# Kernel optimization log

Measured on AMD Instinct MI355X. Metric: run time of the kernel, lower is better.

The kernel has to match this reference:

```python
import jax, jax.numpy as jnp
import numpy as np

B, N, T, FH, H = 4, 5000, 12, 12, 128
DEG = 16
BN = B * N


def setup_inputs():
    key = jax.random.key(0)
    ks = jax.random.split(key, 12)
    rng = np.random.default_rng(0)
    e = N * DEG
    s = rng.integers(0, N, size=(B, e))
    d = rng.integers(0, N, size=(B, e))
    off = (np.arange(B) * N)[:, None]
    edge_index = jnp.asarray(np.stack([(s + off).ravel(), (d + off).ravel()]), dtype=jnp.int32)

    def lin(k, i, o):
        return jax.random.normal(k, (i, o), jnp.float32) / np.sqrt(i).astype(np.float32)

    return {
        "x": jax.random.normal(ks[0], (B, N, T), jnp.float32),
        "gcn_w1": lin(ks[1], 1, 64), "gcn_b1": jnp.zeros(64),
        "gcn_w2": lin(ks[2], 64, H), "gcn_b2": jnp.zeros(H),
        "gcn_w3": lin(ks[3], H, H), "gcn_b3": jnp.zeros(H),
        "att_w1": lin(ks[4], H, H), "att_b1": jnp.zeros(H),
        "att_w2": lin(ks[5], H, 1), "att_b2": jnp.zeros(1),
        "gru_w_ih": jax.random.normal(ks[6], (3 * H, H), jnp.float32) / np.sqrt(H).astype(np.float32),
        "gru_w_hh": jax.random.normal(ks[7], (3 * H, H), jnp.float32) / np.sqrt(H).astype(np.float32),
        "gru_b_ih": jnp.zeros(3 * H), "gru_b_hh": jnp.zeros(3 * H),
        "ode_w1": lin(ks[8], H, H), "ode_b1": jnp.zeros(H),
        "ode_w2": lin(ks[9], H, H), "ode_b2": jnp.zeros(H),
        "out_w": lin(ks[10], H, 1), "out_b": jnp.zeros(1),
        "edge_index": edge_index,
    }


def _forward(x, gcn_w1, gcn_b1, gcn_w2, gcn_b2, gcn_w3, gcn_b3,
             att_w1, att_b1, att_w2, att_b2,
             gru_w_ih, gru_w_hh, gru_b_ih, gru_b_hh,
             ode_w1, ode_b1, ode_w2, ode_b2, out_w, out_b, edge_index):
    # GCNConv with added self-loops and symmetric normalization (PyG semantics)
    loops = jnp.arange(BN, dtype=edge_index.dtype)
    src = jnp.concatenate([edge_index[0], loops])
    dst = jnp.concatenate([edge_index[1], loops])
    deg = jnp.zeros(BN, x.dtype).at[dst].add(1.0)  # >= 1 thanks to self-loops
    dinv = jax.lax.rsqrt(deg)
    norm = (dinv[src] * dinv[dst])[:, None]  # (E+BN, 1)

    def gcn(h, W, b):
        h = h @ W  # (BN, out)
        agg = jnp.zeros((BN, W.shape[1]), h.dtype).at[dst].add(h[src] * norm)
        return agg + b

    # spatial encoder per timestep (scan over the small time axis)
    x_steps = x.reshape(BN, T).T[:, :, None]  # (T, BN, 1)

    def spatial_step(_, x_t):
        h = jax.nn.relu(gcn(x_t, gcn_w1, gcn_b1))
        h = jax.nn.relu(gcn(h, gcn_w2, gcn_b2))
        h = jax.nn.relu(gcn(h, gcn_w3, gcn_b3))
        return None, h

    _, h_seq = jax.lax.scan(spatial_step, None, x_steps)  # (T, BN, H)
    h_seq = h_seq.reshape(T, B, N, H).transpose(1, 0, 2, 3)  # (B, T, N, H)

    # temporal attention over time axis
    att = jnp.tanh(h_seq @ att_w1 + att_b1) @ att_w2 + att_b2  # (B, T, N, 1)
    aw = jax.nn.softmax(att, axis=1)
    node_features = jnp.sum(h_seq * aw, axis=1).reshape(BN, H)

    # single-step GRU with zero initial hidden (torch gate order r, z, n)
    h0 = jnp.zeros((BN, H), x.dtype)
    gi = node_features @ gru_w_ih.T + gru_b_ih
    gh = h0 @ gru_w_hh.T + gru_b_hh
    ir, iz, inn = jnp.split(gi, 3, axis=1)
    hr, hz, hn = jnp.split(gh, 3, axis=1)
    r = jax.nn.sigmoid(ir + hr)
    z = jax.nn.sigmoid(iz + hz)
    n = jnp.tanh(inn + r * hn)
    hidden = (1.0 - z) * n + z * h0  # (BN, H)

    # Graph ODE: dh/dt = tanh(GCN(tanh(GCN(h)))), RK4 on t=linspace(0,FH,FH)
    def ode_f(h):
        h = jnp.tanh(gcn(h, ode_w1, ode_b1))
        return jnp.tanh(gcn(h, ode_w2, ode_b2))

    dt = FH / (FH - 1)

    def rk4(h, _):
        k1 = ode_f(h)
        k2 = ode_f(h + 0.5 * dt * k1)
        k3 = ode_f(h + 0.5 * dt * k2)
        k4 = ode_f(h + dt * k3)
        h2 = h + (dt / 6.0) * (k1 + 2.0 * k2 + 2.0 * k3 + k4)
        return h2, h2

    _, traj = jax.lax.scan(rk4, hidden, None, length=FH - 1)
    states = jnp.concatenate([hidden[None], traj], axis=0)  # (FH, BN, H)
    ev = states.reshape(FH, B, N, H).transpose(1, 2, 0, 3)  # (B, N, FH, H)
    return (ev @ out_w + out_b)[..., 0]  # (B, N, FH)


def reference(x, gcn_w1, gcn_b1, gcn_w2, gcn_b2, gcn_w3, gcn_b3,
              att_w1, att_b1, att_w2, att_b2,
              gru_w_ih, gru_w_hh, gru_b_ih, gru_b_hh,
              ode_w1, ode_b1, ode_w2, ode_b2, out_w, out_b, edge_index):
    return _forward(x, gcn_w1, gcn_b1, gcn_w2, gcn_b2, gcn_w3, gcn_b3,
                    att_w1, att_b1, att_w2, att_b2,
                    gru_w_ih, gru_w_hh, gru_b_ih, gru_b_hh,
                    ode_w1, ode_b1, ode_w2, ode_b2, out_w, out_b, edge_index)
```

## Files before the change

kernel.cpp:

```cpp
#include <hip/hip_runtime.h>
#include <stdint.h>

#define B_ 4
#define N_ 5000
#define T_ 12
#define FH_ 12
#define H_ 128
#define BN_ 20000
#define E_ 320000
#define TOTE_ (E_ + BN_)

typedef __attribute__((ext_vector_type(8))) short s8v;
typedef __attribute__((ext_vector_type(4))) float f32x4;

__device__ __forceinline__ float fast_tanh(float x) {
  float e = __expf(2.f * x);
  return 1.f - 2.f * __builtin_amdgcn_rcpf(e + 1.f);
}
__device__ __forceinline__ float fast_sigmoid(float x) {
  return __builtin_amdgcn_rcpf(1.f + __expf(-x));
}
__device__ __forceinline__ unsigned short f2bf(float f) {
  unsigned u = __float_as_uint(f);
  u = (u + 0x7fffu + ((u >> 16) & 1u)) >> 16;
  return (unsigned short)u;
}
__device__ __forceinline__ float bf2f(unsigned short u) {
  return __uint_as_float(((unsigned)u) << 16);
}
__device__ __forceinline__ unsigned pack2(float lo, float hi) {
  return ((unsigned)f2bf(hi) << 16) | f2bf(lo);
}

__global__ void k_sentinel(float* out) { out[0] = 1e30f; }

__global__ void k_init_cnt(int* cnt) {
  int i = blockIdx.x * 256 + threadIdx.x;
  if (i < BN_) cnt[i] = 1;
}
__global__ void k_count(const int* __restrict__ dst, int* cnt) {
  int e = blockIdx.x * 256 + threadIdx.x;
  if (e < E_) atomicAdd(&cnt[dst[e]], 1);
}
__global__ void k_scan(int* cnt, int* rp, float* dinv) {
  __shared__ int sh[1024];
  int tid = threadIdx.x;
  const int per = (BN_ + 1023) / 1024;
  int start = tid * per;
  int end = start + per; if (end > BN_) end = BN_;
  int s = 0;
  for (int i = start; i < end; i++) {
    int c = cnt[i];
    dinv[i] = rsqrtf((float)c);
    s += c;
  }
  sh[tid] = s;
  __syncthreads();
  for (int off = 1; off < 1024; off <<= 1) {
    int v = (tid >= off) ? sh[tid - off] : 0;
    __syncthreads();
    sh[tid] += v;
    __syncthreads();
  }
  int run = (tid > 0) ? sh[tid - 1] : 0;
  for (int i = start; i < end; i++) {
    int c = cnt[i];
    rp[i] = run;
    run += c;
    cnt[i] = 0;
  }
  if (tid == 1023) rp[BN_] = sh[1023];
}
__global__ void k_fill(const int* __restrict__ src, const int* __restrict__ dst,
                       const int* __restrict__ rp, int* cnt, int2* ev,
                       const float* __restrict__ dinv) {
  int e = blockIdx.x * 256 + threadIdx.x;
  if (e >= TOTE_) return;
  int s, d;
  if (e < E_) { s = src[e]; d = dst[e]; }
  else { s = d = e - E_; }
  int pos = rp[d] + atomicAdd(&cnt[d], 1);
  int2 p; p.x = s; p.y = __float_as_int(dinv[s] * dinv[d]);
  ev[pos] = p;
}

__device__ __forceinline__ void prep_one(const float* __restrict__ src,
                                         unsigned short* __restrict__ dst,
                                         int K, int Nn, int transposed, int idx) {
  int j = idx & 7, l = (idx >> 3) & 63, rest = idx >> 9;
  int NT = Nn >> 4;
  int nt = rest % NT, kc = rest / NT;
  int k = kc * 32 + ((l >> 4) << 3) + j;
  int n = nt * 16 + (l & 15);
  float v = transposed ? src[n * K + k] : src[k * Nn + n];
  dst[idx] = f2bf(v);
}
__global__ void k_prep_all(const float* w2, const float* w3, const float* a1,
                           const float* o1, const float* o2, const float* wih,
                           unsigned short* w2f, unsigned short* w3f, unsigned short* a1f,
                           unsigned short* o1f, unsigned short* o2f, unsigned short* wihf) {
  int idx = blockIdx.x * 256 + threadIdx.x;
  if (idx < 8192) { prep_one(w2, w2f, 64, 128, 0, idx); return; }
  idx -= 8192;
  if (idx < 16384) { prep_one(w3, w3f, 128, 128, 0, idx); return; }
  idx -= 16384;
  if (idx < 16384) { prep_one(a1, a1f, 128, 128, 0, idx); return; }
  idx -= 16384;
  if (idx < 16384) { prep_one(o1, o1f, 128, 128, 0, idx); return; }
  idx -= 16384;
  if (idx < 16384) { prep_one(o2, o2f, 128, 128, 0, idx); return; }
  idx -= 16384;
  if (idx < 49152) prep_one(wih, wihf, 128, 384, 1, idx);
}

__global__ void k_spl1T(const int* __restrict__ rp, const int2* __restrict__ ev,
                        const float* __restrict__ x,
                        const float* __restrict__ w1, const float* __restrict__ b1,
                        unsigned short* __restrict__ h1) {
  int wid = (blockIdx.x * 256 + threadIdx.x) >> 6;
  int lane = threadIdx.x & 63;
  if (wid >= BN_) return;
  int beg = rp[wid], end = rp[wid + 1];
  float a[12];
#pragma unroll
  for (int t = 0; t < 12; t++) a[t] = 0.f;
  for (int e = beg + lane; e < end; e += 64) {
    int2 p = ev[e];
    const float4* xp = (const float4*)(x + (size_t)p.x * 12);
    float v = __int_as_float(p.y);
    float4 x0 = xp[0], x1 = xp[1], x2 = xp[2];
    a[0] = fmaf(v, x0.x, a[0]);  a[1] = fmaf(v, x0.y, a[1]);
    a[2] = fmaf(v, x0.z, a[2]);  a[3] = fmaf(v, x0.w, a[3]);
    a[4] = fmaf(v, x1.x, a[4]);  a[5] = fmaf(v, x1.y, a[5]);
    a[6] = fmaf(v, x1.z, a[6]);  a[7] = fmaf(v, x1.w, a[7]);
    a[8] = fmaf(v, x2.x, a[8]);  a[9] = fmaf(v, x2.y, a[9]);
    a[10] = fmaf(v, x2.z, a[10]); a[11] = fmaf(v, x2.w, a[11]);
  }
#pragma unroll
  for (int t = 0; t < 12; t++)
#pragma unroll
    for (int m = 1; m < 64; m <<= 1) a[t] += __shfl_xor(a[t], m);
  float wv = w1[lane], bv = b1[lane];
#pragma unroll
  for (int t = 0; t < 12; t++) {
    float v = fmaf(a[t], wv, bv);
    h1[((size_t)t * BN_ + wid) * 64 + lane] = f2bf(fmaxf(v, 0.f));
  }
}

template<int KIN>
__device__ __forceinline__ void gather_tile(
    const int* __restrict__ rp, const int2* __restrict__ ev,
    const unsigned short* __restrict__ in, unsigned short (*agg)[KIN + 8],
    int w, int l, int row0g, int nvalid) {
  const int h = l >> 4, c = l & 15;
  constexpr int CW = KIN / 16;
  int start[4], len[4];
  float a[4][CW];
  int mx = 0;
#pragma unroll
  for (int r = 0; r < 4; r++) {
    int lr = w * 4 + r;
    bool ok = lr < nvalid;
    int b0 = ok ? rp[row0g + lr] : 0;
    int e0 = ok ? rp[row0g + lr + 1] : 0;
    int ln = ok ? (e0 - b0) : 0;
    int s0 = (ln * h) >> 2, s1 = (ln * (h + 1)) >> 2;
    start[r] = b0 + s0;
    len[r] = s1 - s0;
    mx = len[r] > mx ? len[r] : mx;
#pragma unroll
    for (int q = 0; q < CW; q++) a[r][q] = 0.f;
  }
  for (int i = 0; i < mx; i++) {
#pragma unroll
    for (int r = 0; r < 4; r++) {
      if (i < len[r]) {
        int2 e = ev[start[r] + i];
        float v = __int_as_float(e.y);
        if (KIN == 128) {
          uint4 p = *(const uint4*)(in + (size_t)e.x * 128 + c * 8);
          a[r][0] = fmaf(v, bf2f((unsigned short)(p.x & 0xffffu)), a[r][0]);
          a[r][1] = fmaf(v, bf2f((unsigned short)(p.x >> 16)), a[r][1]);
          a[r][2] = fmaf(v, bf2f((unsigned short)(p.y & 0xffffu)), a[r][2]);
          a[r][3] = fmaf(v, bf2f((unsigned short)(p.y >> 16)), a[r][3]);
          a[r][4] = fmaf(v, bf2f((unsigned short)(p.z & 0xffffu)), a[r][4]);
          a[r][5] = fmaf(v, bf2f((unsigned short)(p.z >> 16)), a[r][5]);
          a[r][6] = fmaf(v, bf2f((unsigned short)(p.w & 0xffffu)), a[r][6]);
          a[r][7] = fmaf(v, bf2f((unsigned short)(p.w >> 16)), a[r][7]);
        } else {
          uint2 p = *(const uint2*)(in + (size_t)e.x * 64 + c * 4);
          a[r][0] = fmaf(v, bf2f((unsigned short)(p.x & 0xffffu)), a[r][0]);
          a[r][1] = fmaf(v, bf2f((unsigned short)(p.x >> 16)), a[r][1]);
          a[r][2] = fmaf(v, bf2f((unsigned short)(p.y & 0xffffu)), a[r][2]);
          a[r][3] = fmaf(v, bf2f((unsigned short)(p.y >> 16)), a[r][3]);
        }
      }
    }
  }
#pragma unroll
  for (int r = 0; r < 4; r++) {
#pragma unroll
    for (int q = 0; q < CW; q++) {
      a[r][q] += __shfl_xor(a[r][q], 16);
      a[r][q] += __shfl_xor(a[r][q], 32);
    }
    if (h == 0) {
      if (KIN == 128) {
        uint4 o;
        o.x = pack2(a[r][0], a[r][1]); o.y = pack2(a[r][2], a[r][3]);
        o.z = pack2(a[r][4], a[r][5]); o.w = pack2(a[r][6], a[r][7]);
        *(uint4*)&agg[w * 4 + r][c * 8] = o;
      } else {
        uint2 o;
        o.x = pack2(a[r][0], a[r][1]); o.y = pack2(a[r][2], a[r][3]);
        *(uint2*)&agg[w * 4 + r][c * 4] = o;
      }
    }
  }
}

template<int KIN>
__device__ __forceinline__ void mfma_tile(
    const unsigned short (*agg)[KIN + 8], const unsigned short* __restrict__ Wf,
    int w, int l, f32x4 acc[2]) {
  constexpr int KC = KIN / 32;
  const int hi = l >> 4, lo16 = l & 15;
  acc[0] = (f32x4){0.f, 0.f, 0.f, 0.f};
  acc[1] = (f32x4){0.f, 0.f, 0.f, 0.f};
#pragma unroll
  for (int kc = 0; kc < KC; kc++) {
    s8v av = *(const s8v*)&agg[lo16][kc * 32 + hi * 8];
#pragma unroll
    for (int q = 0; q < 2; q++) {
      s8v bv = *(const s8v*)(Wf + (((size_t)(kc * 8 + 2 * w + q)) << 9) + (l << 3));
      acc[q] = __builtin_amdgcn_mfma_f32_16x16x32_bf16(av, bv, acc[q], 0, 0, 0);
    }
  }
}

template<int KIN>
__global__ __launch_bounds__(256) void k_fusedT(
    const int* __restrict__ rp, const int2* __restrict__ ev,
    const unsigned short* __restrict__ inb, const unsigned short* __restrict__ Wf,
    const float* __restrict__ bias, unsigned short* __restrict__ outb) {
  __shared__ unsigned short agg[16][KIN + 8];
  const int tid = threadIdx.x, l = tid & 63, w = tid >> 6;
  const int t = blockIdx.y;
  const unsigned short* in = inb + (size_t)t * BN_ * KIN;
  unsigned short* out = outb + (size_t)t * BN_ * 128;
  const int bid = blockIdx.x;
  const int xcd = bid & 7, slot = bid >> 3;
  const int bb = xcd >> 1;
  const int within = slot * 2 + (xcd & 1);
  const int wr0 = within * 16;
  int nv = N_ - wr0; nv = nv > 16 ? 16 : nv;
  if (nv <= 0) return;
  const int row0g = bb * N_ + wr0;
  gather_tile<KIN>(rp, ev, in, agg, w, l, row0g, nv);
  __syncthreads();
  f32x4 acc[2];
  mfma_tile<KIN>(agg, Wf, w, l, acc);
  const int hi = l >> 4, lo16 = l & 15;
#pragma unroll
  for (int q = 0; q < 2; q++) {
    int col = (2 * w + q) * 16 + lo16;
    float bi = bias[col];
#pragma unroll
    for (int reg = 0; reg < 4; reg++) {
      int lr = hi * 4 + reg;
      if (lr < nv)
        out[(size_t)(row0g + lr) * 128 + col] = f2bf(fmaxf(acc[q][reg] + bi, 0.f));
    }
  }
}

__global__ __launch_bounds__(256) void k_fused(
    const int* __restrict__ rp, const int2* __restrict__ ev,
    const unsigned short* __restrict__ in,
    const unsigned short* __restrict__ Wf, const float* __restrict__ bias,
    int mode, float c1, float c2,
    unsigned short* __restrict__ outb,
    const unsigned short* __restrict__ hbfin, unsigned short* __restrict__ rkb,
    float* __restrict__ h, unsigned short* __restrict__ ubfout,
    const float* __restrict__ ow, const float* __restrict__ ob,
    float* __restrict__ outp, int step) {
  __shared__ unsigned short agg[16][136];
  __shared__ float ppart[4][16];
  const int tid = threadIdx.x, l = tid & 63, w = tid >> 6;
  const int bid = blockIdx.x;
  const int xcd = bid & 7, slot = bid >> 3;
  const int bb = xcd >> 1;
  const int within = slot * 2 + (xcd & 1);
  const int wr0 = within * 16;
  int nv = N_ - wr0; nv = nv > 16 ? 16 : (nv < 0 ? 0 : nv);
  const int row0g = bb * N_ + wr0;
  gather_tile<128>(rp, ev, in, agg, w, l, row0g, nv);
  __syncthreads();
  f32x4 acc[2];
  mfma_tile<128>(agg, Wf, w, l, acc);
  const int hi = l >> 4, lo16 = l & 15;
  float p[4] = {0.f, 0.f, 0.f, 0.f};
#pragma unroll
  for (int q = 0; q < 2; q++) {
    int col = (2 * w + q) * 16 + lo16;
    float bi = bias[col];
    float owv = (mode == 3) ? ow[col] : 0.f;
#pragma unroll
    for (int reg = 0; reg < 4; reg++) {
      int lr = hi * 4 + reg;
      if (lr >= nv) continue;
      size_t oi = (size_t)(row0g + lr) * 128 + col;
      float v = fast_tanh(acc[q][reg] + bi);
      if (mode == 0) {
        outb[oi] = f2bf(v);
      } else if (mode == 1) {
        rkb[oi] = f2bf(v);
        ubfout[oi] = f2bf(fmaf(c1, v, bf2f(hbfin[oi])));
      } else if (mode == 2) {
        rkb[oi] = f2bf(bf2f(rkb[oi]) + 2.f * v);
        ubfout[oi] = f2bf(fmaf(c1, v, bf2f(hbfin[oi])));
      } else {
        float nh = fmaf(c2, bf2f(rkb[oi]) + v, h[oi]);
        h[oi] = nh;
        ubfout[oi] = f2bf(nh);
        p[reg] = fmaf(nh, owv, p[reg]);
      }
    }
  }
  if (mode == 3) {
#pragma unroll
    for (int m = 1; m <= 8; m <<= 1)
#pragma unroll
      for (int reg = 0; reg < 4; reg++) p[reg] += __shfl_xor(p[reg], m);
    if (lo16 == 0)
#pragma unroll
      for (int reg = 0; reg < 4; reg++) ppart[w][hi * 4 + reg] = p[reg];
    __syncthreads();
    if (tid < 16 && tid < nv)
      outp[(size_t)(row0g + tid) * FH_ + step] =
          ppart[0][tid] + ppart[1][tid] + ppart[2][tid] + ppart[3][tid] + ob[0];
  }
}

__global__ __launch_bounds__(256) void k_att(
    const unsigned short* __restrict__ A, const unsigned short* __restrict__ Wf,
    const float* __restrict__ bias, int nrows,
    const float* __restrict__ w2v, const float* __restrict__ b2,
    float* __restrict__ scores) {
  const int tid = threadIdx.x;
  const int l = tid & 63;
  const int w = tid >> 6;
  const int m0 = blockIdx.x * 64 + w * 16;

  f32x4 acc[8];
#pragma unroll
  for (int nt = 0; nt < 8; nt++) acc[nt] = (f32x4){0.f, 0.f, 0.f, 0.f};
  int arow = m0 + (l & 15);
  if (arow >= nrows) arow = nrows - 1;
  const unsigned short* Ap = A + (size_t)arow * 128 + ((l >> 4) << 3);
#pragma unroll
  for (int kc = 0; kc < 4; kc++) {
    s8v av = *(const s8v*)(Ap + kc * 32);
#pragma unroll
    for (int nt = 0; nt < 8; nt++) {
      s8v bv = *(const s8v*)(Wf + (((size_t)(kc * 8 + nt)) << 9) + (l << 3));
      acc[nt] = __builtin_amdgcn_mfma_f32_16x16x32_bf16(av, bv, acc[nt], 0, 0, 0);
    }
  }
  float p[4] = {0.f, 0.f, 0.f, 0.f};
#pragma unroll
  for (int nt = 0; nt < 8; nt++) {
    int col = nt * 16 + (l & 15);
    float bi = bias[col], wv = w2v[col];
#pragma unroll
    for (int reg = 0; reg < 4; reg++)
      p[reg] = fmaf(fast_tanh(acc[nt][reg] + bi), wv, p[reg]);
  }
#pragma unroll
  for (int m = 1; m <= 8; m <<= 1)
#pragma unroll
    for (int reg = 0; reg < 4; reg++) p[reg] += __shfl_xor(p[reg], m);
  if ((l & 15) == 0) {
    float bb = b2[0];
#pragma unroll
    for (int reg = 0; reg < 4; reg++) {
      int row = m0 + ((l >> 4) << 2) + reg;
      if (row < nrows) scores[row] = p[reg] + bb;
    }
  }
}

__global__ void k_attw(const float* __restrict__ sc, const unsigned short* __restrict__ hs,
                       unsigned short* __restrict__ nf) {
  int idx = blockIdx.x * 256 + threadIdx.x;
  if (idx >= BN_ * 64) return;
  int bn = idx >> 6, c = idx & 63;
  float v[T_];
  float m = -1e30f;
#pragma unroll
  for (int t = 0; t < T_; t++) { v[t] = sc[t * BN_ + bn]; m = fmaxf(m, v[t]); }
  float ssum = 0.f;
#pragma unroll
  for (int t = 0; t < T_; t++) { v[t] = __expf(v[t] - m); ssum += v[t]; }
  float inv = __builtin_amdgcn_rcpf(ssum);
  float s0 = 0.f, s1 = 0.f;
#pragma unroll
  for (int t = 0; t < T_; t++) {
    unsigned p = *(const unsigned*)(hs + ((size_t)t * BN_ + bn) * 128 + c * 2);
    float aw = v[t] * inv;
    s0 = fmaf(aw, bf2f((unsigned short)(p & 0xffffu)), s0);
    s1 = fmaf(aw, bf2f((unsigned short)(p >> 16)), s1);
  }
  *(unsigned*)(nf + (size_t)bn * 128 + c * 2) = pack2(s0, s1);
}

__global__ __launch_bounds__(256) void k_gruf(
    const unsigned short* __restrict__ A, const unsigned short* __restrict__ Wf,
    const float* __restrict__ bih, const float* __restrict__ bhh,
    float* __restrict__ hst, unsigned short* __restrict__ hbf,
    const float* __restrict__ ow, const float* __restrict__ ob,
    float* __restrict__ outp) {
  const int tid = threadIdx.x;
  const int l = tid & 63;
  const int w = tid >> 6;
  const int m0 = blockIdx.x * 64 + w * 16;

  f32x4 acc[24];
#pragma unroll
  for (int nt = 0; nt < 24; nt++) acc[nt] = (f32x4){0.f, 0.f, 0.f, 0.f};
  int arow = m0 + (l & 15);
  if (arow >= BN_) arow = BN_ - 1;
  const unsigned short* Ap = A + (size_t)arow * 128 + ((l >> 4) << 3);
#pragma unroll
  for (int kc = 0; kc < 4; kc++) {
    s8v av = *(const s8v*)(Ap + kc * 32);
#pragma unroll
    for (int nt = 0; nt < 24; nt++) {
      s8v bv = *(const s8v*)(Wf + (((size_t)(kc * 24 + nt)) << 9) + (l << 3));
      acc[nt] = __builtin_amdgcn_mfma_f32_16x16x32_bf16(av, bv, acc[nt], 0, 0, 0);
    }
  }
  const int hi = l >> 4, lo16 = l & 15;
  float p[4] = {0.f, 0.f, 0.f, 0.f};
#pragma unroll
  for (int nt = 0; nt < 8; nt++) {
    int col = nt * 16 + lo16;
    float br = bih[col], bz = bih[col + 128], bn = bih[col + 256];
    float hr = bhh[col], hz = bhh[col + 128], hn = bhh[col + 256];
    float owv = ow[col];
#pragma unroll
    for (int reg = 0; reg < 4; reg++) {
      int row = m0 + hi * 4 + reg;
      if (row >= BN_) continue;
      float r = fast_sigmoid(acc[nt][reg] + br + hr);
      float z = fast_sigmoid(acc[nt + 8][reg] + bz + hz);
      float n = fast_tanh(acc[nt + 16][reg] + bn + r * hn);
      float hv = (1.f - z) * n;
      size_t oi = (size_t)row * 128 + col;
      hst[oi] = hv;
      hbf[oi] = f2bf(hv);
      p[reg] = fmaf(hv, owv, p[reg]);
    }
  }
#pragma unroll
  for (int m = 1; m <= 8; m <<= 1)
#pragma unroll
    for (int reg = 0; reg < 4; reg++) p[reg] += __shfl_xor(p[reg], m);
  if (lo16 == 0) {
    float obv = ob[0];
#pragma unroll
    for (int reg = 0; reg < 4; reg++) {
      int row = m0 + hi * 4 + reg;
      if (row < BN_) outp[(size_t)row * FH_ + 0] = p[reg] + obv;
    }
  }
}

extern "C" void kernel_launch(void* const* d_in, const int* in_sizes, int n_in,
                              void* d_out, int out_size, void* d_ws, size_t ws_size,
                              hipStream_t stream) {
  const float* x       = (const float*)d_in[0];
  const float* gcn_w1  = (const float*)d_in[1];
  const float* gcn_b1  = (const float*)d_in[2];
  const float* gcn_w2  = (const float*)d_in[3];
  const float* gcn_b2  = (const float*)d_in[4];
  const float* gcn_w3  = (const float*)d_in[5];
  const float* gcn_b3  = (const float*)d_in[6];
  const float* att_w1  = (const float*)d_in[7];
  const float* att_b1  = (const float*)d_in[8];
  const float* att_w2  = (const float*)d_in[9];
  const float* att_b2  = (const float*)d_in[10];
  const float* gru_wih = (const float*)d_in[11];
  const float* gru_bih = (const float*)d_in[13];
  const float* gru_bhh = (const float*)d_in[14];
  const float* ode_w1  = (const float*)d_in[15];
  const float* ode_b1  = (const float*)d_in[16];
  const float* ode_w2  = (const float*)d_in[17];
  const float* ode_b2  = (const float*)d_in[18];
  const float* out_w   = (const float*)d_in[19];
  const float* out_b   = (const float*)d_in[20];
  const int*   eidx    = (const int*)d_in[21];
  float* out = (float*)d_out;

  float* wsf = (float*)d_ws;
  size_t off = 0;
  unsigned short* h1b12 = (unsigned short*)(wsf + off); off += (size_t)BN_ * 384;
  float* hst    = wsf + off; off += (size_t)BN_ * H_;
  float* scores = wsf + off; off += (size_t)T_ * BN_;
  float* dinv   = wsf + off; off += BN_;
  int2*  ev     = (int2*)(wsf + off); off += (size_t)TOTE_ * 2;
  unsigned short* hseqb  = (unsigned short*)(wsf + off); off += (size_t)T_ * BN_ * H_ / 2;
  unsigned short* t1b12  = (unsigned short*)(wsf + off); off += (size_t)T_ * BN_ * H_ / 2;
  unsigned short* hbf    = (unsigned short*)(wsf + off); off += (size_t)BN_ * H_ / 2;
  unsigned short* ubf    = (unsigned short*)(wsf + off); off += (size_t)BN_ * H_ / 2;
  unsigned short* rkb    = (unsigned short*)(wsf + off); off += (size_t)BN_ * H_ / 2;
  unsigned short* nfbf   = (unsigned short*)(wsf + off); off += (size_t)BN_ * H_ / 2;
  unsigned short* w2f    = (unsigned short*)(wsf + off); off += 64 * 128 / 2;
  unsigned short* w3f    = (unsigned short*)(wsf + off); off += 128 * 128 / 2;
  unsigned short* aw1f   = (unsigned short*)(wsf + off); off += 128 * 128 / 2;
  unsigned short* ow1f   = (unsigned short*)(wsf + off); off += 128 * 128 / 2;
  unsigned short* ow2f   = (unsigned short*)(wsf + off); off += 128 * 128 / 2;
  unsigned short* wihf   = (unsigned short*)(wsf + off); off += 128 * 384 / 2;
  int* rp  = (int*)(wsf + off); off += BN_ + 1;
  int* cnt = (int*)(wsf + off); off += BN_;
  if (ws_size < off * sizeof(float)) {
    k_sentinel<<<1, 1, 0, stream>>>(out);
    return;
  }

  const int* esrc = eidx;
  const int* edst = eidx + E_;

  k_init_cnt<<<(BN_ + 255) / 256, 256, 0, stream>>>(cnt);
  k_count<<<(E_ + 255) / 256, 256, 0, stream>>>(edst, cnt);
  k_scan<<<1, 1024, 0, stream>>>(cnt, rp, dinv);
  k_fill<<<(TOTE_ + 255) / 256, 256, 0, stream>>>(esrc, edst, rp, cnt, ev, dinv);
  k_prep_all<<<480, 256, 0, stream>>>(gcn_w2, gcn_w3, att_w1, ode_w1, ode_w2, gru_wih,
                                      w2f, w3f, aw1f, ow1f, ow2f, wihf);

  const int gW = BN_ / 4;
  const int gR = (BN_ + 63) / 64;
  const int gF = 1280;

  k_spl1T<<<gW, 256, 0, stream>>>(rp, ev, x, gcn_w1, gcn_b1, h1b12);
  k_fusedT<64><<<dim3(gF, 12), 256, 0, stream>>>(rp, ev, h1b12, w2f, gcn_b2, t1b12);
  k_fusedT<128><<<dim3(gF, 12), 256, 0, stream>>>(rp, ev, t1b12, w3f, gcn_b3, hseqb);

  k_att<<<(T_ * BN_ + 63) / 64, 256, 0, stream>>>(hseqb, aw1f, att_b1, T_ * BN_,
                                                  att_w2, att_b2, scores);
  k_attw<<<(BN_ * 64 + 255) / 256, 256, 0, stream>>>(scores, hseqb, nfbf);

  k_gruf<<<gR, 256, 0, stream>>>(nfbf, wihf, gru_bih, gru_bhh, hst, hbf,
                                 out_w, out_b, out);

  const float dt = (float)FH_ / (float)(FH_ - 1);
  unsigned short* t1 = t1b12;
  auto f_eval = [&](const unsigned short* inbf, int mode, float c1, float c2, int step) {
    k_fused<<<gF, 256, 0, stream>>>(rp, ev, inbf, ow1f, ode_b1, 0, 0.f, 0.f,
                                    t1, nullptr, nullptr, nullptr, nullptr,
                                    nullptr, nullptr, nullptr, 0);
    k_fused<<<gF, 256, 0, stream>>>(rp, ev, t1, ow2f, ode_b2, mode, c1, c2,
                                    nullptr, hbf, rkb, hst,
                                    (mode == 3) ? hbf : ubf,
                                    out_w, out_b, out, step);
  };
  for (int s = 1; s < FH_; s++) {
    f_eval(hbf, 1, 0.5f * dt, 0.f, s);
    f_eval(ubf, 2, 0.5f * dt, 0.f, s);
    f_eval(ubf, 2, dt, 0.f, s);
    f_eval(ubf, 3, 0.f, dt / 6.f, s);
  }
}
```

Baseline: 2.121 ms.

## Pad CSR rows to pairs, pre-scale indices, and sort rows by degree

Pads each CSR row to an even length, using zeroed padding entries, so the gather loop reads two edges per 16-byte load and issues two feature loads per iteration. Source indices are stored pre-multiplied by 128 to drop address arithmetic. Rows are reordered by a per-batch degree histogram so each 16-row tile groups nodes with similar degree, which reduces load imbalance across warps. In exchange it adds setup kernels and memsets, writes outputs through an indirection, and makes padded rows gather node 0 with zero weight.

```diff
diff --git a/kernel.cpp b/kernel.cpp
--- a/kernel.cpp
+++ b/kernel.cpp
@@ -9,6 +9,7 @@
 #define BN_ 20000
 #define E_ 320000
 #define TOTE_ (E_ + BN_)
+#define EVCAP_ (TOTE_ + BN_)
 
 typedef __attribute__((ext_vector_type(8))) short s8v;
 typedef __attribute__((ext_vector_type(4))) float f32x4;
@@ -52,7 +53,7 @@
   for (int i = start; i < end; i++) {
     int c = cnt[i];
     dinv[i] = rsqrtf((float)c);
-    s += c;
+    s += (c + 1) & ~1;
   }
   sh[tid] = s;
   __syncthreads();
@@ -66,7 +67,7 @@
   for (int i = start; i < end; i++) {
     int c = cnt[i];
     rp[i] = run;
-    run += c;
+    run += (c + 1) & ~1;
     cnt[i] = 0;
   }
   if (tid == 1023) rp[BN_] = sh[1023];
@@ -80,8 +81,38 @@
   if (e < E_) { s = src[e]; d = dst[e]; }
   else { s = d = e - E_; }
   int pos = rp[d] + atomicAdd(&cnt[d], 1);
-  int2 p; p.x = s; p.y = __float_as_int(dinv[s] * dinv[d]);
+  int2 p; p.x = s * 128; p.y = __float_as_int(dinv[s] * dinv[d]);
   ev[pos] = p;
+}
+
+__global__ void k_hist(const int* __restrict__ rp, int* hist) {
+  int i = blockIdx.x * 256 + threadIdx.x;
+  if (i < BN_) {
+    int d = rp[i + 1] - rp[i]; d = d > 63 ? 63 : d;
+    atomicAdd(&hist[(i / N_) * 64 + d], 1);
+  }
+}
+__global__ void k_binscan(int* hist) {
+  __shared__ int sh[256];
+  int t = threadIdx.x;
+  int val = hist[t];
+  sh[t] = val;
+  __syncthreads();
+  for (int o = 1; o < 256; o <<= 1) {
+    int v = (t >= o) ? sh[t - o] : 0;
+    __syncthreads();
+    sh[t] += v;
+    __syncthreads();
+  }
+  hist[t] = sh[t] - val;
+}
+__global__ void k_scatter(const int* __restrict__ rp, int* hist, int* ord) {
+  int i = blockIdx.x * 256 + threadIdx.x;
+  if (i < BN_) {
+    int d = rp[i + 1] - rp[i]; d = d > 63 ? 63 : d;
+    int pos = atomicAdd(&hist[(i / N_) * 64 + d], 1);
+    ord[pos] = i;
+  }
 }
 
 __device__ __forceinline__ void prep_one(const float* __restrict__ src,
@@ -126,7 +157,7 @@
   for (int t = 0; t < 12; t++) a[t] = 0.f;
   for (int e = beg + lane; e < end; e += 64) {
     int2 p = ev[e];
-    const float4* xp = (const float4*)(x + (size_t)p.x * 12);
+    const float4* xp = (const float4*)(x + (size_t)(p.x >> 7) * 12);
     float v = __int_as_float(p.y);
     float4 x0 = xp[0], x1 = xp[1], x2 = xp[2];
     a[0] = fmaf(v, x0.x, a[0]);  a[1] = fmaf(v, x0.y, a[1]);
@@ -152,48 +183,65 @@
 __device__ __forceinline__ void gather_tile(
     const int* __restrict__ rp, const int2* __restrict__ ev,
     const unsigned short* __restrict__ in, unsigned short (*agg)[KIN + 8],
-    int w, int l, int row0g, int nvalid) {
+    const int* __restrict__ ordt, int w, int l, int nvalid) {
   const int h = l >> 4, c = l & 15;
   constexpr int CW = KIN / 16;
-  int start[4], len[4];
+  const unsigned short* inc = in + c * CW;
+  int st[4], len[4];
   float a[4][CW];
   int mx = 0;
 #pragma unroll
   for (int r = 0; r < 4; r++) {
     int lr = w * 4 + r;
     bool ok = lr < nvalid;
-    int b0 = ok ? rp[row0g + lr] : 0;
-    int e0 = ok ? rp[row0g + lr + 1] : 0;
-    int ln = ok ? (e0 - b0) : 0;
-    int s0 = (ln * h) >> 2, s1 = (ln * (h + 1)) >> 2;
-    start[r] = b0 + s0;
-    len[r] = s1 - s0;
+    int row = ok ? ordt[lr] : 0;
+    int b0 = ok ? rp[row] : 0;
+    int e0 = ok ? rp[row + 1] : 0;
+    int np = (e0 - b0) >> 1;
+    int p0 = (np * h) >> 2, p1 = (np * (h + 1)) >> 2;
+    st[r] = (b0 >> 1) + p0;
+    len[r] = p1 - p0;
     mx = len[r] > mx ? len[r] : mx;
 #pragma unroll
     for (int q = 0; q < CW; q++) a[r][q] = 0.f;
   }
+  const int4* evp = (const int4*)ev;
   for (int i = 0; i < mx; i++) {
 #pragma unroll
     for (int r = 0; r < 4; r++) {
       if (i < len[r]) {
-        int2 e = ev[start[r] + i];
-        float v = __int_as_float(e.y);
+        int4 q = evp[st[r] + i];
+        float v0 = __int_as_float(q.y), v1 = __int_as_float(q.w);
         if (KIN == 128) {
-          uint4 p = *(const uint4*)(in + (size_t)e.x * 128 + c * 8);
-          a[r][0] = fmaf(v, bf2f((unsigned short)(p.x & 0xffffu)), a[r][0]);
-          a[r][1] = fmaf(v, bf2f((unsigned short)(p.x >> 16)), a[r][1]);
-          a[r][2] = fmaf(v, bf2f((unsigned short)(p.y & 0xffffu)), a[r][2]);
-          a[r][3] = fmaf(v, bf2f((unsigned short)(p.y >> 16)), a[r][3]);
-          a[r][4] = fmaf(v, bf2f((unsigned short)(p.z & 0xffffu)), a[r][4]);
-          a[r][5] = fmaf(v, bf2f((unsigned short)(p.z >> 16)), a[r][5]);
-          a[r][6] = fmaf(v, bf2f((unsigned short)(p.w & 0xffffu)), a[r][6]);
-          a[r][7] = fmaf(v, bf2f((unsigned short)(p.w >> 16)), a[r][7]);
+          uint4 pA = *(const uint4*)(inc + q.x);
+          uint4 pB = *(const uint4*)(inc + q.z);
+          a[r][0] = fmaf(v0, bf2f((unsigned short)(pA.x & 0xffffu)), a[r][0]);
+          a[r][1] = fmaf(v0, bf2f((unsigned short)(pA.x >> 16)), a[r][1]);
+          a[r][2] = fmaf(v0, bf2f((unsigned short)(pA.y & 0xffffu)), a[r][2]);
+          a[r][3] = fmaf(v0, bf2f((unsigned short)(pA.y >> 16)), a[r][3]);
+          a[r][4] = fmaf(v0, bf2f((unsigned short)(pA.z & 0xffffu)), a[r][4]);
+          a[r][5] = fmaf(v0, bf2f((unsigned short)(pA.z >> 16)), a[r][5]);
+          a[r][6] = fmaf(v0, bf2f((unsigned short)(pA.w & 0xffffu)), a[r][6]);
+          a[r][7] = fmaf(v0, bf2f((unsigned short)(pA.w >> 16)), a[r][7]);
+          a[r][0] = fmaf(v1, bf2f((unsigned short)(pB.x & 0xffffu)), a[r][0]);
+          a[r][1] = fmaf(v1, bf2f((unsigned short)(pB.x >> 16)), a[r][1]);
+          a[r][2] = fmaf(v1, bf2f((unsigned short)(pB.y & 0xffffu)), a[r][2]);
+          a[r][3] = fmaf(v1, bf2f((unsigned short)(pB.y >> 16)), a[r][3]);
+          a[r][4] = fmaf(v1, bf2f((unsigned short)(pB.z & 0xffffu)), a[r][4]);
+          a[r][5] = fmaf(v1, bf2f((unsigned short)(pB.z >> 16)), a[r][5]);
+          a[r][6] = fmaf(v1, bf2f((unsigned short)(pB.w & 0xffffu)), a[r][6]);
+          a[r][7] = fmaf(v1, bf2f((unsigned short)(pB.w >> 16)), a[r][7]);
         } else {
-          uint2 p = *(const uint2*)(in + (size_t)e.x * 64 + c * 4);
-          a[r][0] = fmaf(v, bf2f((unsigned short)(p.x & 0xffffu)), a[r][0]);
-          a[r][1] = fmaf(v, bf2f((unsigned short)(p.x >> 16)), a[r][1]);
-          a[r][2] = fmaf(v, bf2f((unsigned short)(p.y & 0xffffu)), a[r][2]);
-          a[r][3] = fmaf(v, bf2f((unsigned short)(p.y >> 16)), a[r][3]);
+          uint2 pA = *(const uint2*)(inc + (q.x >> 1));
+          uint2 pB = *(const uint2*)(inc + (q.z >> 1));
+          a[r][0] = fmaf(v0, bf2f((unsigned short)(pA.x & 0xffffu)), a[r][0]);
+          a[r][1] = fmaf(v0, bf2f((unsigned short)(pA.x >> 16)), a[r][1]);
+          a[r][2] = fmaf(v0, bf2f((unsigned short)(pA.y & 0xffffu)), a[r][2]);
+          a[r][3] = fmaf(v0, bf2f((unsigned short)(pA.y >> 16)), a[r][3]);
+          a[r][0] = fmaf(v1, bf2f((unsigned short)(pB.x & 0xffffu)), a[r][0]);
+          a[r][1] = fmaf(v1, bf2f((unsigned short)(pB.x >> 16)), a[r][1]);
+          a[r][2] = fmaf(v1, bf2f((unsigned short)(pB.y & 0xffffu)), a[r][2]);
+          a[r][3] = fmaf(v1, bf2f((unsigned short)(pB.y >> 16)), a[r][3]);
         }
       }
     }
@@ -242,6 +290,7 @@
 template<int KIN>
 __global__ __launch_bounds__(256) void k_fusedT(
     const int* __restrict__ rp, const int2* __restrict__ ev,
+    const int* __restrict__ ord,
     const unsigned short* __restrict__ inb, const unsigned short* __restrict__ Wf,
     const float* __restrict__ bias, unsigned short* __restrict__ outb) {
   __shared__ unsigned short agg[16][KIN + 8];
@@ -256,8 +305,8 @@
   const int wr0 = within * 16;
   int nv = N_ - wr0; nv = nv > 16 ? 16 : nv;
   if (nv <= 0) return;
-  const int row0g = bb * N_ + wr0;
-  gather_tile<KIN>(rp, ev, in, agg, w, l, row0g, nv);
+  const int* ordt = ord + bb * N_ + wr0;
+  gather_tile<KIN>(rp, ev, in, agg, ordt, w, l, nv);
   __syncthreads();
   f32x4 acc[2];
   mfma_tile<KIN>(agg, Wf, w, l, acc);
@@ -269,14 +318,17 @@
 #pragma unroll
     for (int reg = 0; reg < 4; reg++) {
       int lr = hi * 4 + reg;
-      if (lr < nv)
-        out[(size_t)(row0g + lr) * 128 + col] = f2bf(fmaxf(acc[q][reg] + bi, 0.f));
+      if (lr < nv) {
+        int grow = ordt[lr];
+        out[(size_t)grow * 128 + col] = f2bf(fmaxf(acc[q][reg] + bi, 0.f));
+      }
     }
   }
 }
 
 __global__ __launch_bounds__(256) void k_fused(
     const int* __restrict__ rp, const int2* __restrict__ ev,
+    const int* __restrict__ ord,
     const unsigned short* __restrict__ in,
     const unsigned short* __restrict__ Wf, const float* __restrict__ bias,
     int mode, float c1, float c2,
@@ -294,8 +346,9 @@
   const int within = slot * 2 + (xcd & 1);
   const int wr0 = within * 16;
   int nv = N_ - wr0; nv = nv > 16 ? 16 : (nv < 0 ? 0 : nv);
-  const int row0g = bb * N_ + wr0;
-  gather_tile<128>(rp, ev, in, agg, w, l, row0g, nv);
+  if (nv <= 0) return;
+  const int* ordt = ord + bb * N_ + wr0;
+  gather_tile<128>(rp, ev, in, agg, ordt, w, l, nv);
   __syncthreads();
   f32x4 acc[2];
   mfma_tile<128>(agg, Wf, w, l, acc);
@@ -310,7 +363,8 @@
     for (int reg = 0; reg < 4; reg++) {
       int lr = hi * 4 + reg;
       if (lr >= nv) continue;
-      size_t oi = (size_t)(row0g + lr) * 128 + col;
+      int grow = ordt[lr];
+      size_t oi = (size_t)grow * 128 + col;
       float v = fast_tanh(acc[q][reg] + bi);
       if (mode == 0) {
         outb[oi] = f2bf(v);
@@ -337,9 +391,11 @@
 #pragma unroll
       for (int reg = 0; reg < 4; reg++) ppart[w][hi * 4 + reg] = p[reg];
     __syncthreads();
-    if (tid < 16 && tid < nv)
-      outp[(size_t)(row0g + tid) * FH_ + step] =
+    if (tid < 16 && tid < nv) {
+      int grow = ordt[tid];
+      outp[(size_t)grow * FH_ + step] =
           ppart[0][tid] + ppart[1][tid] + ppart[2][tid] + ppart[3][tid] + ob[0];
+    }
   }
 }
 
@@ -509,7 +565,7 @@
   float* hst    = wsf + off; off += (size_t)BN_ * H_;
   float* scores = wsf + off; off += (size_t)T_ * BN_;
   float* dinv   = wsf + off; off += BN_;
-  int2*  ev     = (int2*)(wsf + off); off += (size_t)TOTE_ * 2;
+  int2*  ev     = (int2*)(wsf + off); off += (size_t)EVCAP_ * 2;
   unsigned short* hseqb  = (unsigned short*)(wsf + off); off += (size_t)T_ * BN_ * H_ / 2;
   unsigned short* t1b12  = (unsigned short*)(wsf + off); off += (size_t)T_ * BN_ * H_ / 2;
   unsigned short* hbf    = (unsigned short*)(wsf + off); off += (size_t)BN_ * H_ / 2;
@@ -522,8 +578,10 @@
   unsigned short* ow1f   = (unsigned short*)(wsf + off); off += 128 * 128 / 2;
   unsigned short* ow2f   = (unsigned short*)(wsf + off); off += 128 * 128 / 2;
   unsigned short* wihf   = (unsigned short*)(wsf + off); off += 128 * 384 / 2;
-  int* rp  = (int*)(wsf + off); off += BN_ + 1;
-  int* cnt = (int*)(wsf + off); off += BN_;
+  int* rp   = (int*)(wsf + off); off += BN_ + 1;
+  int* cnt  = (int*)(wsf + off); off += BN_;
+  int* ord  = (int*)(wsf + off); off += BN_;
+  int* hist = (int*)(wsf + off); off += 256;
   if (ws_size < off * sizeof(float)) {
     k_sentinel<<<1, 1, 0, stream>>>(out);
     return;
@@ -531,11 +589,17 @@
 
   const int* esrc = eidx;
   const int* edst = eidx + E_;
-
-  k_init_cnt<<<(BN_ + 255) / 256, 256, 0, stream>>>(cnt);
+  const int g79 = (BN_ + 255) / 256;
+
+  hipMemsetAsync(ev, 0, (size_t)EVCAP_ * sizeof(int2), stream);
+  hipMemsetAsync(hist, 0, 256 * sizeof(int), stream);
+  k_init_cnt<<<g79, 256, 0, stream>>>(cnt);
   k_count<<<(E_ + 255) / 256, 256, 0, stream>>>(edst, cnt);
   k_scan<<<1, 1024, 0, stream>>>(cnt, rp, dinv);
   k_fill<<<(TOTE_ + 255) / 256, 256, 0, stream>>>(esrc, edst, rp, cnt, ev, dinv);
+  k_hist<<<g79, 256, 0, stream>>>(rp, hist);
+  k_binscan<<<1, 256, 0, stream>>>(hist);
+  k_scatter<<<g79, 256, 0, stream>>>(rp, hist, ord);
   k_prep_all<<<480, 256, 0, stream>>>(gcn_w2, gcn_w3, att_w1, ode_w1, ode_w2, gru_wih,
                                       w2f, w3f, aw1f, ow1f, ow2f, wihf);
 
@@ -544,8 +608,8 @@
   const int gF = 1280;
 
   k_spl1T<<<gW, 256, 0, stream>>>(rp, ev, x, gcn_w1, gcn_b1, h1b12);
-  k_fusedT<64><<<dim3(gF, 12), 256, 0, stream>>>(rp, ev, h1b12, w2f, gcn_b2, t1b12);
-  k_fusedT<128><<<dim3(gF, 12), 256, 0, stream>>>(rp, ev, t1b12, w3f, gcn_b3, hseqb);
+  k_fusedT<64><<<dim3(gF, 12), 256, 0, stream>>>(rp, ev, ord, h1b12, w2f, gcn_b2, t1b12);
+  k_fusedT<128><<<dim3(gF, 12), 256, 0, stream>>>(rp, ev, ord, t1b12, w3f, gcn_b3, hseqb);
 
   k_att<<<(T_ * BN_ + 63) / 64, 256, 0, stream>>>(hseqb, aw1f, att_b1, T_ * BN_,
                                                   att_w2, att_b2, scores);
@@ -557,10 +621,10 @@
   const float dt = (float)FH_ / (float)(FH_ - 1);
   unsigned short* t1 = t1b12;
   auto f_eval = [&](const unsigned short* inbf, int mode, float c1, float c2, int step) {
-    k_fused<<<gF, 256, 0, stream>>>(rp, ev, inbf, ow1f, ode_b1, 0, 0.f, 0.f,
+    k_fused<<<gF, 256, 0, stream>>>(rp, ev, ord, inbf, ow1f, ode_b1, 0, 0.f, 0.f,
                                     t1, nullptr, nullptr, nullptr, nullptr,
                                     nullptr, nullptr, nullptr, 0);
-    k_fused<<<gF, 256, 0, stream>>>(rp, ev, t1, ow2f, ode_b2, mode, c1, c2,
+    k_fused<<<gF, 256, 0, stream>>>(rp, ev, ord, t1, ow2f, ode_b2, mode, c1, c2,
                                     nullptr, hbf, rkb, hst,
                                     (mode == 3) ? hbf : ubf,
                                     out_w, out_b, out, step);
```

Result: faster. 2.048 ms (-3.4%).
